# Kernel optimization log

Hardware: AMD Instinct MI355X
Metric: run time of the kernel (lower is better)

## Reference

```python
import jax, jax.numpy as jnp
import numpy as np

B, N, CQ, CKV, CP = 4, 1024, 128, 64, 16
H, NB = 4, 3
D = CQ // H  # 32 per-head dim
NQ, NK = 32, 128
CENTRES = 15.5 + 32.0 * np.arange(N // NQ)  # subset centres covering all atoms


def _ln(x, eps=1e-5):
    m = jnp.mean(x, axis=-1, keepdims=True)
    v = jnp.var(x, axis=-1, keepdims=True)
    return (x - m) * jax.lax.rsqrt(v + eps)


def _adaln(a, s, s_gamma, w_gate, w_skip):
    # AF3 AdaLN: a normalized without affine, modulated by conditioning s
    a_n = _ln(a)
    s_n = _ln(s) * s_gamma
    return jax.nn.sigmoid(s_n @ w_gate) * a_n + s_n @ w_skip


def _local_bias():
    # sequence-local block mask (union over subset centres), Algorithm 7
    idx = jnp.arange(N, dtype=jnp.float32)
    cen = jnp.asarray(CENTRES, dtype=jnp.float32)
    lcond = jnp.abs(idx[None, :] - cen[:, None]) < NQ / 2  # [C, N] query window
    mcond = jnp.abs(idx[None, :] - cen[:, None]) < NK / 2  # [C, N] key window
    cond = jnp.any(lcond[:, :, None] & mcond[:, None, :], axis=0)  # [N, N]
    return jnp.where(cond, 0.0, -1e10)


def _forward(q, c, p, attn_s_gamma, attn_gate_w, attn_skip_w, attn_wq, attn_bq,
             attn_wk, attn_wv, attn_lnz_g, attn_lnz_b, attn_wb, attn_wgate,
             attn_wo, attn_ws_out, attn_bs_out, trans_s_gamma, trans_gate_w,
             trans_skip_w, trans_w1, trans_w2, trans_wout, trans_ws_out,
             trans_bs_out):
    beta = _local_bias()  # [N, N]
    inv_sqrt_d = 1.0 / np.sqrt(D)
    a = q
    for i in range(NB):  # 3 structurally distinct blocks
        # --- AttentionPairBias (AF3 Alg 24) ---
        ah = _adaln(a, c, attn_s_gamma[i], attn_gate_w[i], attn_skip_w[i])
        qh = (ah @ attn_wq[i] + attn_bq[i]).reshape(B, N, H, D)
        kh = (ah @ attn_wk[i]).reshape(B, N, H, D)
        vh = (ah @ attn_wv[i]).reshape(B, N, H, D)
        zb = (_ln(p) * attn_lnz_g[i] + attn_lnz_b[i]) @ attn_wb[i]  # [B,N,N,H]
        bias = jnp.transpose(zb, (0, 3, 1, 2)) + beta[None, None]  # [B,H,N,N]
        scores = jnp.einsum('bqhd,bkhd->bhqk', qh, kh) * inv_sqrt_d + bias
        w = jax.nn.softmax(scores, axis=-1)
        o = jnp.einsum('bhqk,bkhd->bqhd', w, vh)
        g = jax.nn.sigmoid((ah @ attn_wgate[i]).reshape(B, N, H, D))
        o = (g * o).reshape(B, N, CQ) @ attn_wo[i]
        attn_out = jax.nn.sigmoid(c @ attn_ws_out[i] + attn_bs_out[i]) * o
        # --- ConditionedTransitionBlock (AF3 Alg 25, n=2 SwiGLU) ---
        t = _adaln(a, c, trans_s_gamma[i], trans_gate_w[i], trans_skip_w[i])
        bm = jax.nn.silu(t @ trans_w1[i]) * (t @ trans_w2[i])
        t_out = jax.nn.sigmoid(c @ trans_ws_out[i] + trans_bs_out[i]) * (bm @ trans_wout[i])
        # AF3 Alg 23: a <- attn_out + transition(a, s)
        a = attn_out + t_out
    return a


def setup_inputs() -> dict:
    key = jax.random.key(0)
    ks = iter(jax.random.split(key, 64))

    def rnd(shape, scale=0.02):
        return jax.random.normal(next(ks), shape, dtype=jnp.float32) * scale

    return {
        'q': jax.random.normal(next(ks), (B, N, CQ), dtype=jnp.float32),
        'c': jax.random.normal(next(ks), (B, N, CKV), dtype=jnp.float32),
        'p': jax.random.normal(next(ks), (B, N, N, CP), dtype=jnp.float32),
        'attn_s_gamma': jnp.ones((NB, CKV), jnp.float32),
        'attn_gate_w': rnd((NB, CKV, CQ)),
        'attn_skip_w': rnd((NB, CKV, CQ)),
        'attn_wq': rnd((NB, CQ, CQ)),
        'attn_bq': jnp.zeros((NB, CQ), jnp.float32),
        'attn_wk': rnd((NB, CQ, CQ)),
        'attn_wv': rnd((NB, CQ, CQ)),
        'attn_lnz_g': jnp.ones((NB, CP), jnp.float32),
        'attn_lnz_b': jnp.zeros((NB, CP), jnp.float32),
        'attn_wb': rnd((NB, CP, H)),
        'attn_wgate': rnd((NB, CQ, CQ)),
        'attn_wo': rnd((NB, CQ, CQ)),
        'attn_ws_out': rnd((NB, CKV, CQ)),
        'attn_bs_out': jnp.full((NB, CQ), -2.0, jnp.float32),
        'trans_s_gamma': jnp.ones((NB, CKV), jnp.float32),
        'trans_gate_w': rnd((NB, CKV, CQ)),
        'trans_skip_w': rnd((NB, CKV, CQ)),
        'trans_w1': rnd((NB, CQ, 2 * CQ)),
        'trans_w2': rnd((NB, CQ, 2 * CQ)),
        'trans_wout': rnd((NB, 2 * CQ, CQ)),
        'trans_ws_out': rnd((NB, CKV, CQ)),
        'trans_bs_out': jnp.full((NB, CQ), -2.0, jnp.float32),
    }


def reference(q, c, p, attn_s_gamma, attn_gate_w, attn_skip_w, attn_wq, attn_bq,
              attn_wk, attn_wv, attn_lnz_g, attn_lnz_b, attn_wb, attn_wgate,
              attn_wo, attn_ws_out, attn_bs_out, trans_s_gamma, trans_gate_w,
              trans_skip_w, trans_w1, trans_w2, trans_wout, trans_ws_out,
              trans_bs_out):
    return _forward(q, c, p, attn_s_gamma, attn_gate_w, attn_skip_w, attn_wq,
                    attn_bq, attn_wk, attn_wv, attn_lnz_g, attn_lnz_b, attn_wb,
                    attn_wgate, attn_wo, attn_ws_out, attn_bs_out,
                    trans_s_gamma, trans_gate_w, trans_skip_w, trans_w1,
                    trans_w2, trans_wout, trans_ws_out, trans_bs_out)
```

## Files before the change

### kernel.cpp

```cpp
#include <hip/hip_runtime.h>
#include <math.h>

#define NB_ 3
#define B_ 4
#define N_ 1024
#define CQ_ 128
#define CKV_ 64
#define CP_ 16
#define H_ 4
#define D_ 32
#define R_ (B_*N_)
#define KW_ 128

__device__ __forceinline__ float sigmoidf_(float x) {
    return 1.0f / (1.0f + __expf(-x));
}

#define AN_OFF 0
#define SA_OFF 1056
#define ST_OFF 1600
#define CR_OFF 2144
#define TH_OFF 2688
#define SCR_OFF 3744
#define SMEM_F (3744 + 6336)

__device__ __forceinline__ void pre_body(
    float2 av, float* smem, int base,
    const float* __restrict__ c,
    const float* __restrict__ a_sg, const float* __restrict__ a_gw,
    const float* __restrict__ a_sw, const float* __restrict__ a_wso,
    const float* __restrict__ a_bso,
    const float* __restrict__ t_sg, const float* __restrict__ t_gw,
    const float* __restrict__ t_sw, const float* __restrict__ t_wso,
    const float* __restrict__ t_bso,
    const float* __restrict__ wq, const float* __restrict__ bq,
    const float* __restrict__ wk, const float* __restrict__ wv,
    const float* __restrict__ wg,
    const float* __restrict__ w1, const float* __restrict__ w2,
    float* __restrict__ qh, float* __restrict__ kh,
    float* __restrict__ vh, float* __restrict__ gh,
    float* __restrict__ bm,
    float* __restrict__ asig, float* __restrict__ tsig)
{
    const int t = threadIdx.x;
    {
        const int rloc = t >> 6, li = t & 63;
        const int row = base + rloc;
        float s = av.x + av.y;
        float ss = av.x * av.x + av.y * av.y;
        float cv = c[row * 64 + li];
        float cs = cv, css = cv * cv;
        #pragma unroll
        for (int m = 1; m < 64; m <<= 1) {
            s += __shfl_xor(s, m);
            ss += __shfl_xor(ss, m);
            cs += __shfl_xor(cs, m);
            css += __shfl_xor(css, m);
        }
        const float am = s * (1.0f / 128.0f);
        const float ars = rsqrtf(ss * (1.0f / 128.0f) - am * am + 1e-5f);
        const float cm = cs * (1.0f / 64.0f);
        const float crs = rsqrtf(css * (1.0f / 64.0f) - cm * cm + 1e-5f);
        smem[AN_OFF + rloc * 132 + li * 2]     = (av.x - am) * ars;
        smem[AN_OFF + rloc * 132 + li * 2 + 1] = (av.y - am) * ars;
        const float cn = (cv - cm) * crs;
        smem[SA_OFF + rloc * 68 + li] = cn * a_sg[li];
        smem[ST_OFF + rloc * 68 + li] = cn * t_sg[li];
        smem[CR_OFF + rloc * 68 + li] = cv;
    }
    __syncthreads();

    const int wave = t >> 6;
    const int lane = t & 63;
    const int ig = lane >> 4;
    const int jc = lane & 15;
    const int c0 = jc * 8;
    const int r0 = ig * 2, r1 = ig * 2 + 1;

    if (wave < 6) {
        const float* W;
        const float* xs;
        switch (wave) {
            case 0: W = a_gw;  xs = smem + SA_OFF; break;
            case 1: W = a_sw;  xs = smem + SA_OFF; break;
            case 2: W = t_gw;  xs = smem + ST_OFF; break;
            case 3: W = t_sw;  xs = smem + ST_OFF; break;
            case 4: W = a_wso; xs = smem + CR_OFF; break;
            default: W = t_wso; xs = smem + CR_OFF; break;
        }
        W += c0;
        float acc0[8], acc1[8];
        #pragma unroll
        for (int e = 0; e < 8; e++) { acc0[e] = 0.f; acc1[e] = 0.f; }
        for (int kk = 0; kk < 64; kk += 4) {
            float4 x40 = *(const float4*)(xs + r0 * 68 + kk);
            float4 x41 = *(const float4*)(xs + r1 * 68 + kk);
            #pragma unroll
            for (int qq = 0; qq < 4; qq++) {
                const float4 wlo = *(const float4*)(W + (kk + qq) * 128);
                const float4 whi = *(const float4*)(W + (kk + qq) * 128 + 4);
                const float xa = ((const float*)&x40)[qq];
                const float xb = ((const float*)&x41)[qq];
                acc0[0] += xa * wlo.x; acc0[1] += xa * wlo.y;
                acc0[2] += xa * wlo.z; acc0[3] += xa * wlo.w;
                acc0[4] += xa * whi.x; acc0[5] += xa * whi.y;
                acc0[6] += xa * whi.z; acc0[7] += xa * whi.w;
                acc1[0] += xb * wlo.x; acc1[1] += xb * wlo.y;
                acc1[2] += xb * wlo.z; acc1[3] += xb * wlo.w;
                acc1[4] += xb * whi.x; acc1[5] += xb * whi.y;
                acc1[6] += xb * whi.z; acc1[7] += xb * whi.w;
            }
        }
        float* sc = smem + SCR_OFF + wave * 1056;
        *(float4*)(sc + r0 * 132 + c0)     = make_float4(acc0[0], acc0[1], acc0[2], acc0[3]);
        *(float4*)(sc + r0 * 132 + c0 + 4) = make_float4(acc0[4], acc0[5], acc0[6], acc0[7]);
        *(float4*)(sc + r1 * 132 + c0)     = make_float4(acc1[0], acc1[1], acc1[2], acc1[3]);
        *(float4*)(sc + r1 * 132 + c0 + 4) = make_float4(acc1[4], acc1[5], acc1[6], acc1[7]);
    }
    __syncthreads();

    #pragma unroll
    for (int i2 = 0; i2 < 2; i2++) {
        const int e = t + i2 * 512;
        const int r = e >> 7, cc = e & 127;
        const float* sc = smem + SCR_OFF + r * 132 + cc;
        const float anv = smem[AN_OFF + r * 132 + cc];
        const float ahv = sigmoidf_(sc[0]) * anv + sc[1056];
        const float thv = sigmoidf_(sc[2 * 1056]) * anv + sc[3 * 1056];
        smem[AN_OFF + r * 132 + cc] = ahv;
        smem[TH_OFF + r * 132 + cc] = thv;
        const int idx = (base + r) * 128 + cc;
        asig[idx] = sigmoidf_(sc[4 * 1056] + a_bso[cc]);
        tsig[idx] = sigmoidf_(sc[5 * 1056] + t_bso[cc]);
    }
    __syncthreads();

    {
        const float* W;
        const float* xs;
        int ldw, sel2 = 0, cb = 0;
        if (wave < 4) {
            W = (wave == 0 ? wq : wave == 1 ? wk : wave == 2 ? wv : wg) + c0;
            xs = smem + AN_OFF;
            ldw = 128;
        } else {
            const int u = (wave - 4) * 128 + c0;
            sel2 = u >> 8; cb = u & 255;
            W = (sel2 ? w2 : w1) + cb;
            xs = smem + TH_OFF;
            ldw = 256;
        }
        float acc0[8], acc1[8];
        #pragma unroll
        for (int e = 0; e < 8; e++) {
            const float init = (wave == 0) ? bq[c0 + e] : 0.f;
            acc0[e] = init; acc1[e] = init;
        }
        for (int kk = 0; kk < 128; kk += 4) {
            float4 x40 = *(const float4*)(xs + r0 * 132 + kk);
            float4 x41 = *(const float4*)(xs + r1 * 132 + kk);
            #pragma unroll
            for (int qq = 0; qq < 4; qq++) {
                const float4 wlo = *(const float4*)(W + (kk + qq) * ldw);
                const float4 whi = *(const float4*)(W + (kk + qq) * ldw + 4);
                const float xa = ((const float*)&x40)[qq];
                const float xb = ((const float*)&x41)[qq];
                acc0[0] += xa * wlo.x; acc0[1] += xa * wlo.y;
                acc0[2] += xa * wlo.z; acc0[3] += xa * wlo.w;
                acc0[4] += xa * whi.x; acc0[5] += xa * whi.y;
                acc0[6] += xa * whi.z; acc0[7] += xa * whi.w;
                acc1[0] += xb * wlo.x; acc1[1] += xb * wlo.y;
                acc1[2] += xb * wlo.z; acc1[3] += xb * wlo.w;
                acc1[4] += xb * whi.x; acc1[5] += xb * whi.y;
                acc1[6] += xb * whi.z; acc1[7] += xb * whi.w;
            }
        }
        if (wave < 4) {
            float* dst = (wave == 0 ? qh : wave == 1 ? kh : wave == 2 ? vh : gh);
            if (wave == 3) {
                #pragma unroll
                for (int e = 0; e < 8; e++) {
                    acc0[e] = sigmoidf_(acc0[e]);
                    acc1[e] = sigmoidf_(acc1[e]);
                }
            }
            *(float4*)(dst + (base + r0) * 128 + c0)     = make_float4(acc0[0], acc0[1], acc0[2], acc0[3]);
            *(float4*)(dst + (base + r0) * 128 + c0 + 4) = make_float4(acc0[4], acc0[5], acc0[6], acc0[7]);
            *(float4*)(dst + (base + r1) * 128 + c0)     = make_float4(acc1[0], acc1[1], acc1[2], acc1[3]);
            *(float4*)(dst + (base + r1) * 128 + c0 + 4) = make_float4(acc1[4], acc1[5], acc1[6], acc1[7]);
        } else {
            float* bsc = smem + SCR_OFF + sel2 * 2080;
            *(float4*)(bsc + r0 * 260 + cb)     = make_float4(acc0[0], acc0[1], acc0[2], acc0[3]);
            *(float4*)(bsc + r0 * 260 + cb + 4) = make_float4(acc0[4], acc0[5], acc0[6], acc0[7]);
            *(float4*)(bsc + r1 * 260 + cb)     = make_float4(acc1[0], acc1[1], acc1[2], acc1[3]);
            *(float4*)(bsc + r1 * 260 + cb + 4) = make_float4(acc1[4], acc1[5], acc1[6], acc1[7]);
        }
    }
    __syncthreads();

    #pragma unroll
    for (int i2 = 0; i2 < 4; i2++) {
        const int e = t + i2 * 512;
        const int r = e >> 8, cc = e & 255;
        const float a1 = smem[SCR_OFF + r * 260 + cc];
        const float a2 = smem[SCR_OFF + 2080 + r * 260 + cc];
        bm[(base + r) * 256 + cc] = a1 * sigmoidf_(a1) * a2;
    }
}

__global__ __launch_bounds__(512, 4) void k_pre0(
    const float* __restrict__ a, const float* __restrict__ c,
    const float* __restrict__ p,
    const float* __restrict__ lnz_g, const float* __restrict__ lnz_b,
    const float* __restrict__ wb, float* __restrict__ zb,
    const float* __restrict__ a_sg, const float* __restrict__ a_gw,
    const float* __restrict__ a_sw, const float* __restrict__ a_wso,
    const float* __restrict__ a_bso,
    const float* __restrict__ t_sg, const float* __restrict__ t_gw,
    const float* __restrict__ t_sw, const float* __restrict__ t_wso,
    const float* __restrict__ t_bso,
    const float* __restrict__ wq, const float* __restrict__ bq,
    const float* __restrict__ wk, const float* __restrict__ wv,
    const float* __restrict__ wg,
    const float* __restrict__ w1, const float* __restrict__ w2,
    float* __restrict__ qh, float* __restrict__ kh,
    float* __restrict__ vh, float* __restrict__ gh,
    float* __restrict__ bm,
    float* __restrict__ asig, float* __restrict__ tsig)
{
    __shared__ float smem[SMEM_F];
    const int t = threadIdx.x;
    const int base = blockIdx.x * 8;

    #pragma unroll
    for (int i = 0; i < 2; i++) {
        const int e = t + i * 512;
        const int r = e >> 7, kk = e & 127;
        const int row = base + r;
        const int n = row & 1023;
        const int k = ((n >> 5) << 5) - 48 + kk;
        if (k < 0 || k >= N_) {
            #pragma unroll
            for (int blk = 0; blk < NB_; blk++) {
                float* zo = zb + ((size_t)(blk * R_ + row) * H_) * KW_ + kk;
                #pragma unroll
                for (int h = 0; h < H_; h++) zo[h * KW_] = -1e10f;
            }
        } else {
            const float* pp = p + ((size_t)row * N_ + k) * CP_;
            float pv[16];
            float4 p0 = *(const float4*)(pp);
            float4 p1 = *(const float4*)(pp + 4);
            float4 p2 = *(const float4*)(pp + 8);
            float4 p3 = *(const float4*)(pp + 12);
            pv[0]=p0.x; pv[1]=p0.y; pv[2]=p0.z; pv[3]=p0.w;
            pv[4]=p1.x; pv[5]=p1.y; pv[6]=p1.z; pv[7]=p1.w;
            pv[8]=p2.x; pv[9]=p2.y; pv[10]=p2.z; pv[11]=p2.w;
            pv[12]=p3.x; pv[13]=p3.y; pv[14]=p3.z; pv[15]=p3.w;
            float s = 0.f, ss = 0.f;
            #pragma unroll
            for (int ii = 0; ii < 16; ii++) { s += pv[ii]; ss += pv[ii] * pv[ii]; }
            const float m = s * (1.0f / 16.0f);
            const float rs = rsqrtf(ss * (1.0f / 16.0f) - m * m + 1e-5f);
            #pragma unroll
            for (int blk = 0; blk < NB_; blk++) {
                const float* g = lnz_g + blk * 16;
                const float* bb = lnz_b + blk * 16;
                const float* w = wb + blk * 64;
                float z0 = 0.f, z1 = 0.f, z2 = 0.f, z3 = 0.f;
                #pragma unroll
                for (int cp = 0; cp < 16; cp++) {
                    const float val = (pv[cp] - m) * rs * g[cp] + bb[cp];
                    z0 += val * w[cp * 4 + 0];
                    z1 += val * w[cp * 4 + 1];
                    z2 += val * w[cp * 4 + 2];
                    z3 += val * w[cp * 4 + 3];
                }
                float* zo = zb + ((size_t)(blk * R_ + row) * H_) * KW_ + kk;
                zo[0] = z0; zo[KW_] = z1; zo[2 * KW_] = z2; zo[3 * KW_] = z3;
            }
        }
    }

    float2 av = *(const float2*)(a + (base + (t >> 6)) * 128 + (t & 63) * 2);
    pre_body(av, smem, base, c, a_sg, a_gw, a_sw, a_wso, a_bso,
             t_sg, t_gw, t_sw, t_wso, t_bso, wq, bq, wk, wv, wg, w1, w2,
             qh, kh, vh, gh, bm, asig, tsig);
}

__global__ __launch_bounds__(512, 4) void k_cp(
    const float* __restrict__ og, const float* __restrict__ bm_in,
    const float* __restrict__ wo, const float* __restrict__ wout,
    const float* __restrict__ asig_in, const float* __restrict__ tsig_in,
    float* __restrict__ out_final, int final_,
    const float* __restrict__ c,
    const float* __restrict__ a_sg, const float* __restrict__ a_gw,
    const float* __restrict__ a_sw, const float* __restrict__ a_wso,
    const float* __restrict__ a_bso,
    const float* __restrict__ t_sg, const float* __restrict__ t_gw,
    const float* __restrict__ t_sw, const float* __restrict__ t_wso,
    const float* __restrict__ t_bso,
    const float* __restrict__ wq, const float* __restrict__ bq,
    const float* __restrict__ wk, const float* __restrict__ wv,
    const float* __restrict__ wg,
    const float* __restrict__ w1, const float* __restrict__ w2,
    float* __restrict__ qh, float* __restrict__ kh,
    float* __restrict__ vh, float* __restrict__ gh,
    float* __restrict__ bm,
    float* __restrict__ asig, float* __restrict__ tsig)
{
    __shared__ float smem[SMEM_F];
    float* ogs = smem + SCR_OFF;
    float* bms = smem + SCR_OFF + 1056;
    const int t = threadIdx.x;
    const int base = blockIdx.x * 8;

    if (t < 256) {
        const int r = t >> 5, c4 = t & 31;
        *(float4*)(ogs + r * 132 + c4 * 4) =
            *(const float4*)(og + (base + r) * 128 + c4 * 4);
    }
    {
        const int r = t >> 6, c4 = t & 63;
        *(float4*)(bms + r * 260 + c4 * 4) =
            *(const float4*)(bm_in + (base + r) * 256 + c4 * 4);
    }
    __syncthreads();

    const int w = t >> 6, l = t & 63;
    const int row = base + w;
    float2 acc1 = make_float2(0.f, 0.f), acc2 = make_float2(0.f, 0.f);
    for (int k = 0; k < 128; k++) {
        const float x = ogs[w * 132 + k];
        const float2 wv = *(const float2*)(wo + k * 128 + l * 2);
        acc1.x += x * wv.x; acc1.y += x * wv.y;
    }
    for (int k = 0; k < 256; k++) {
        const float x = bms[w * 260 + k];
        const float2 wv = *(const float2*)(wout + k * 128 + l * 2);
        acc2.x += x * wv.x; acc2.y += x * wv.y;
    }
    const float2 as = *(const float2*)(asig_in + row * 128 + l * 2);
    const float2 ts = *(const float2*)(tsig_in + row * 128 + l * 2);
    float2 outv;
    outv.x = as.x * acc1.x + ts.x * acc2.x;
    outv.y = as.y * acc1.y + ts.y * acc2.y;

    if (final_) {
        *(float2*)(out_final + row * 128 + l * 2) = outv;
        return;
    }
    pre_body(outv, smem, base, c, a_sg, a_gw, a_sw, a_wso, a_bso,
             t_sg, t_gw, t_sw, t_wso, t_bso, wq, bq, wk, wv, wg, w1, w2,
             qh, kh, vh, gh, bm, asig, tsig);
}

__global__ __launch_bounds__(512, 4) void k_attn(
    const float* __restrict__ qh, const float* __restrict__ kh,
    const float* __restrict__ vh, const float* __restrict__ gh,
    const float* __restrict__ zb, float* __restrict__ og)
{
    __shared__ float qs[32 * 36];
    __shared__ float kT[32 * 136];
    __shared__ float vs[128 * 36];
    __shared__ float wsm[32 * 132];

    const int t = threadIdx.x;
    const int qb = blockIdx.x & 31;
    const int h = (blockIdx.x >> 5) & 3;
    const int b = blockIdx.x >> 7;
    const int k0 = qb * 32 - 48;

    #pragma unroll
    for (int i = 0; i < 2; i++) {
        const int e = t + i * 512;
        const int kk = e >> 3, dq = e & 7;
        const int kg = k0 + kk;
        float4 kv = make_float4(0.f, 0.f, 0.f, 0.f);
        float4 vv = make_float4(0.f, 0.f, 0.f, 0.f);
        if (kg >= 0 && kg < N_) {
            const int addr = (b * N_ + kg) * 128 + h * 32 + dq * 4;
            kv = *(const float4*)(kh + addr);
            vv = *(const float4*)(vh + addr);
        }
        kT[(dq * 4 + 0) * 136 + kk] = kv.x;
        kT[(dq * 4 + 1) * 136 + kk] = kv.y;
        kT[(dq * 4 + 2) * 136 + kk] = kv.z;
        kT[(dq * 4 + 3) * 136 + kk] = kv.w;
        *(float4*)(vs + kk * 36 + dq * 4) = vv;
    }
    if (t < 256) {
        const int q = t >> 3, dq = t & 7;
        const int n = qb * 32 + q;
        *(float4*)(qs + q * 36 + dq * 4) =
            *(const float4*)(qh + (b * N_ + n) * 128 + h * 32 + dq * 4);
    }
    const int q = t >> 4, jj = t & 15;
    const int n = qb * 32 + q;
    const float* zrow = zb + ((size_t)(b * N_ + n) * H_ + h) * KW_;
    const float4 z0 = *(const float4*)(zrow + jj * 8);
    const float4 z1 = *(const float4*)(zrow + jj * 8 + 4);
    __syncthreads();

    float acc[8];
    #pragma unroll
    for (int e = 0; e < 8; e++) acc[e] = 0.f;
    for (int d = 0; d < 32; d++) {
        const float qv = qs[q * 36 + d];
        const float4 ka = *(const float4*)(kT + d * 136 + jj * 8);
        const float4 kb = *(const float4*)(kT + d * 136 + jj * 8 + 4);
        acc[0] += qv * ka.x; acc[1] += qv * ka.y;
        acc[2] += qv * ka.z; acc[3] += qv * ka.w;
        acc[4] += qv * kb.x; acc[5] += qv * kb.y;
        acc[6] += qv * kb.z; acc[7] += qv * kb.w;
    }
    const float scale = 0.1767766952966369f;
    float fr[8];
    fr[0] = acc[0] * scale + z0.x; fr[1] = acc[1] * scale + z0.y;
    fr[2] = acc[2] * scale + z0.z; fr[3] = acc[3] * scale + z0.w;
    fr[4] = acc[4] * scale + z1.x; fr[5] = acc[5] * scale + z1.y;
    fr[6] = acc[6] * scale + z1.z; fr[7] = acc[7] * scale + z1.w;
    float mx = fr[0];
    #pragma unroll
    for (int i = 1; i < 8; i++) mx = fmaxf(mx, fr[i]);
    #pragma unroll
    for (int mk = 1; mk < 16; mk <<= 1) mx = fmaxf(mx, __shfl_xor(mx, mk));
    float sum = 0.f;
    #pragma unroll
    for (int i = 0; i < 8; i++) { fr[i] = __expf(fr[i] - mx); sum += fr[i]; }
    #pragma unroll
    for (int mk = 1; mk < 16; mk <<= 1) sum += __shfl_xor(sum, mk);
    const float rinv = 1.0f / sum;
    #pragma unroll
    for (int i = 0; i < 8; i++)
        wsm[q * 132 + jj * 8 + i] = fr[i] * rinv;
    __syncthreads();

    const int q2 = t >> 4, dq2 = (t >> 1) & 7, kh2 = t & 1;
    float4 o = make_float4(0.f, 0.f, 0.f, 0.f);
    const int kbeg = kh2 * 64;
    for (int kk = kbeg; kk < kbeg + 64; kk++) {
        const float wv = wsm[q2 * 132 + kk];
        const float4 v4 = *(const float4*)(vs + kk * 36 + dq2 * 4);
        o.x += wv * v4.x; o.y += wv * v4.y;
        o.z += wv * v4.z; o.w += wv * v4.w;
    }
    o.x += __shfl_xor(o.x, 1);
    o.y += __shfl_xor(o.y, 1);
    o.z += __shfl_xor(o.z, 1);
    o.w += __shfl_xor(o.w, 1);
    if (kh2 == 0) {
        const int n2 = qb * 32 + q2;
        const int addr = (b * N_ + n2) * 128 + h * 32 + dq2 * 4;
        const float4 g4 = *(const float4*)(gh + addr);
        float4 outv;
        outv.x = o.x * g4.x; outv.y = o.y * g4.y;
        outv.z = o.z * g4.z; outv.w = o.w * g4.w;
        *(float4*)(og + addr) = outv;
    }
}

extern "C" void kernel_launch(void* const* d_in, const int* in_sizes, int n_in,
                              void* d_out, int out_size, void* d_ws, size_t ws_size,
                              hipStream_t stream)
{
    const float* q        = (const float*)d_in[0];
    const float* c        = (const float*)d_in[1];
    const float* p        = (const float*)d_in[2];
    const float* a_sg_all = (const float*)d_in[3];
    const float* a_gw_all = (const float*)d_in[4];
    const float* a_sw_all = (const float*)d_in[5];
    const float* wq_all   = (const float*)d_in[6];
    const float* bq_all   = (const float*)d_in[7];
    const float* wk_all   = (const float*)d_in[8];
    const float* wv_all   = (const float*)d_in[9];
    const float* lnzg_all = (const float*)d_in[10];
    const float* lnzb_all = (const float*)d_in[11];
    const float* wb_all   = (const float*)d_in[12];
    const float* wgt_all  = (const float*)d_in[13];
    const float* wo_all   = (const float*)d_in[14];
    const float* awso_all = (const float*)d_in[15];
    const float* abso_all = (const float*)d_in[16];
    const float* t_sg_all = (const float*)d_in[17];
    const float* t_gw_all = (const float*)d_in[18];
    const float* t_sw_all = (const float*)d_in[19];
    const float* w1_all   = (const float*)d_in[20];
    const float* w2_all   = (const float*)d_in[21];
    const float* wout_all = (const float*)d_in[22];
    const float* twso_all = (const float*)d_in[23];
    const float* tbso_all = (const float*)d_in[24];

    float* ws = (float*)d_ws;
    const size_t RC = (size_t)R_ * CQ_;
    float* qh   = ws;
    float* kh   = ws + RC;
    float* vh   = ws + 2 * RC;
    float* gh   = ws + 3 * RC;
    float* bmb  = ws + 4 * RC;
    float* asig = ws + 6 * RC;
    float* tsig = ws + 7 * RC;
    float* ogb  = ws + 8 * RC;
    float* zbb  = ws + 9 * RC;

    k_pre0<<<dim3(R_ / 8), dim3(512), 0, stream>>>(
        q, c, p, lnzg_all, lnzb_all, wb_all, zbb,
        a_sg_all, a_gw_all, a_sw_all, awso_all, abso_all,
        t_sg_all, t_gw_all, t_sw_all, twso_all, tbso_all,
        wq_all, bq_all, wk_all, wv_all, wgt_all, w1_all, w2_all,
        qh, kh, vh, gh, bmb, asig, tsig);

    for (int blk = 0; blk < NB_; blk++) {
        k_attn<<<dim3(512), dim3(512), 0, stream>>>(
            qh, kh, vh, gh, zbb + (size_t)blk * R_ * H_ * KW_, ogb);
        const int nxt = blk + 1;
        const int fin = (nxt == NB_);
        const int wi = fin ? 0 : nxt;
        k_cp<<<dim3(R_ / 8), dim3(512), 0, stream>>>(
            ogb, bmb, wo_all + blk * CQ_ * CQ_, wout_all + blk * 2 * CQ_ * CQ_,
            asig, tsig, (float*)d_out, fin,
            c,
            a_sg_all + wi * CKV_, a_gw_all + wi * CKV_ * CQ_,
            a_sw_all + wi * CKV_ * CQ_, awso_all + wi * CKV_ * CQ_,
            abso_all + wi * CQ_,
            t_sg_all + wi * CKV_, t_gw_all + wi * CKV_ * CQ_,
            t_sw_all + wi * CKV_ * CQ_, twso_all + wi * CKV_ * CQ_,
            tbso_all + wi * CQ_,
            wq_all + wi * CQ_ * CQ_, bq_all + wi * CQ_,
            wk_all + wi * CQ_ * CQ_, wv_all + wi * CQ_ * CQ_,
            wgt_all + wi * CQ_ * CQ_,
            w1_all + wi * CQ_ * 2 * CQ_, w2_all + wi * CQ_ * 2 * CQ_,
            qh, kh, vh, gh, bmb, asig, tsig);
    }
}
```

Baseline: 686.4 us.

## Fuse all stages into one persistent kernel with software grid barriers

Replaces the seven separate launches (pre, then attention and combine per block) with a single persistent kernel of 256 workgroups. The workgroups synchronise through an atomic counter used as a grid barrier, and the q/k/v/g buffers are double-buffered so the next block's projections can be written while others still read. Each workgroup now handles 16 rows and two attention tiles, and the combine GEMM splits its K dimension across waves. This removes per-launch overhead and inter-kernel gaps, but the barriers need every workgroup resident at once, and the smaller grid may lose parallelism.

```diff
diff --git a/kernel.cpp b/kernel.cpp
--- a/kernel.cpp
+++ b/kernel.cpp
@@ -8,9 +8,9 @@
 #define CKV_ 64
 #define CP_ 16
 #define H_ 4
-#define D_ 32
 #define R_ (B_*N_)
 #define KW_ 128
+#define NBLK 256
 
 __device__ __forceinline__ float sigmoidf_(float x) {
     return 1.0f / (1.0f + __expf(-x));
@@ -22,7 +22,26 @@
 #define CR_OFF 2144
 #define TH_OFF 2688
 #define SCR_OFF 3744
-#define SMEM_F (3744 + 6336)
+#define AOUT_OFF 10080
+#define QS_OFF 0
+#define KT_OFF 1152
+#define VS_OFF 5504
+#define WS_OFF 10112
+#define SMEM_F 14336
+
+__device__ __forceinline__ void grid_barrier(unsigned* bar, unsigned target) {
+    __syncthreads();
+    if (threadIdx.x == 0) {
+        __builtin_amdgcn_fence(__ATOMIC_RELEASE, "agent");
+        __hip_atomic_fetch_add(bar, 1u, __ATOMIC_ACQ_REL, __HIP_MEMORY_SCOPE_AGENT);
+        while (__hip_atomic_load(bar, __ATOMIC_RELAXED,
+                                 __HIP_MEMORY_SCOPE_AGENT) < target) {
+            __builtin_amdgcn_s_sleep(2);
+        }
+        __builtin_amdgcn_fence(__ATOMIC_ACQUIRE, "agent");
+    }
+    __syncthreads();
+}
 
 __device__ __forceinline__ void pre_body(
     float2 av, float* smem, int base,
@@ -206,37 +225,231 @@
         const float a2 = smem[SCR_OFF + 2080 + r * 260 + cc];
         bm[(base + r) * 256 + cc] = a1 * sigmoidf_(a1) * a2;
     }
+    __syncthreads();
 }
 
-__global__ __launch_bounds__(512, 4) void k_pre0(
-    const float* __restrict__ a, const float* __restrict__ c,
+__device__ __forceinline__ void attn_body(
+    float* smem, int tile,
+    const float* __restrict__ qh, const float* __restrict__ kh,
+    const float* __restrict__ vh, const float* __restrict__ gh,
+    const float* __restrict__ zb, float* __restrict__ og)
+{
+    float* qs = smem + QS_OFF;
+    float* kT = smem + KT_OFF;
+    float* vs = smem + VS_OFF;
+    float* wsm = smem + WS_OFF;
+    const int t = threadIdx.x;
+    const int qb = tile & 31;
+    const int h = (tile >> 5) & 3;
+    const int b = tile >> 7;
+    const int k0 = qb * 32 - 48;
+
+    #pragma unroll
+    for (int i = 0; i < 2; i++) {
+        const int e = t + i * 512;
+        const int kk = e >> 3, dq = e & 7;
+        const int kg = k0 + kk;
+        float4 kv = make_float4(0.f, 0.f, 0.f, 0.f);
+        float4 vv = make_float4(0.f, 0.f, 0.f, 0.f);
+        if (kg >= 0 && kg < N_) {
+            const int addr = (b * N_ + kg) * 128 + h * 32 + dq * 4;
+            kv = *(const float4*)(kh + addr);
+            vv = *(const float4*)(vh + addr);
+        }
+        kT[(dq * 4 + 0) * 136 + kk] = kv.x;
+        kT[(dq * 4 + 1) * 136 + kk] = kv.y;
+        kT[(dq * 4 + 2) * 136 + kk] = kv.z;
+        kT[(dq * 4 + 3) * 136 + kk] = kv.w;
+        *(float4*)(vs + kk * 36 + dq * 4) = vv;
+    }
+    if (t < 256) {
+        const int q = t >> 3, dq = t & 7;
+        const int n = qb * 32 + q;
+        *(float4*)(qs + q * 36 + dq * 4) =
+            *(const float4*)(qh + (b * N_ + n) * 128 + h * 32 + dq * 4);
+    }
+    const int q = t >> 4, jj = t & 15;
+    const int n = qb * 32 + q;
+    const float* zrow = zb + ((size_t)(b * N_ + n) * H_ + h) * KW_;
+    const float4 z0 = *(const float4*)(zrow + jj * 8);
+    const float4 z1 = *(const float4*)(zrow + jj * 8 + 4);
+    __syncthreads();
+
+    float acc[8];
+    #pragma unroll
+    for (int e = 0; e < 8; e++) acc[e] = 0.f;
+    for (int d = 0; d < 32; d++) {
+        const float qv = qs[q * 36 + d];
+        const float4 ka = *(const float4*)(kT + d * 136 + jj * 8);
+        const float4 kb = *(const float4*)(kT + d * 136 + jj * 8 + 4);
+        acc[0] += qv * ka.x; acc[1] += qv * ka.y;
+        acc[2] += qv * ka.z; acc[3] += qv * ka.w;
+        acc[4] += qv * kb.x; acc[5] += qv * kb.y;
+        acc[6] += qv * kb.z; acc[7] += qv * kb.w;
+    }
+    const float scale = 0.1767766952966369f;
+    float fr[8];
+    fr[0] = acc[0] * scale + z0.x; fr[1] = acc[1] * scale + z0.y;
+    fr[2] = acc[2] * scale + z0.z; fr[3] = acc[3] * scale + z0.w;
+    fr[4] = acc[4] * scale + z1.x; fr[5] = acc[5] * scale + z1.y;
+    fr[6] = acc[6] * scale + z1.z; fr[7] = acc[7] * scale + z1.w;
+    float mx = fr[0];
+    #pragma unroll
+    for (int i = 1; i < 8; i++) mx = fmaxf(mx, fr[i]);
+    #pragma unroll
+    for (int mk = 1; mk < 16; mk <<= 1) mx = fmaxf(mx, __shfl_xor(mx, mk));
+    float sum = 0.f;
+    #pragma unroll
+    for (int i = 0; i < 8; i++) { fr[i] = __expf(fr[i] - mx); sum += fr[i]; }
+    #pragma unroll
+    for (int mk = 1; mk < 16; mk <<= 1) sum += __shfl_xor(sum, mk);
+    const float rinv = 1.0f / sum;
+    #pragma unroll
+    for (int i = 0; i < 8; i++)
+        wsm[q * 132 + jj * 8 + i] = fr[i] * rinv;
+    __syncthreads();
+
+    const int q2 = t >> 4, dq2 = (t >> 1) & 7, kh2 = t & 1;
+    float4 o = make_float4(0.f, 0.f, 0.f, 0.f);
+    const int kbeg = kh2 * 64;
+    for (int kk = kbeg; kk < kbeg + 64; kk++) {
+        const float wv = wsm[q2 * 132 + kk];
+        const float4 v4 = *(const float4*)(vs + kk * 36 + dq2 * 4);
+        o.x += wv * v4.x; o.y += wv * v4.y;
+        o.z += wv * v4.z; o.w += wv * v4.w;
+    }
+    o.x += __shfl_xor(o.x, 1);
+    o.y += __shfl_xor(o.y, 1);
+    o.z += __shfl_xor(o.z, 1);
+    o.w += __shfl_xor(o.w, 1);
+    if (kh2 == 0) {
+        const int n2 = qb * 32 + q2;
+        const int addr = (b * N_ + n2) * 128 + h * 32 + dq2 * 4;
+        const float4 g4 = *(const float4*)(gh + addr);
+        float4 outv;
+        outv.x = o.x * g4.x; outv.y = o.y * g4.y;
+        outv.z = o.z * g4.z; outv.w = o.w * g4.w;
+        *(float4*)(og + addr) = outv;
+    }
+    __syncthreads();
+}
+
+__device__ __forceinline__ void combine16(
+    float* smem, int base16,
+    const float* __restrict__ og, const float* __restrict__ bmg,
+    const float* __restrict__ wo, const float* __restrict__ wout,
+    const float* __restrict__ asig, const float* __restrict__ tsig,
+    float* __restrict__ outp)
+{
+    const int t = threadIdx.x;
+    const int grp = t >> 8;
+    const int tg = t & 255;
+    const int base8 = base16 + grp * 8;
+    float* scr = smem + grp * 4224;
+    const int wave = tg >> 6, lane = tg & 63;
+    const int ig = lane >> 4, jc = lane & 15;
+    const int c0 = jc * 8;
+    const int r0 = ig * 2, r1 = ig * 2 + 1;
+
+    float acc0[8], acc1[8];
+    #pragma unroll
+    for (int e = 0; e < 8; e++) { acc0[e] = 0.f; acc1[e] = 0.f; }
+
+    if (wave < 2) {
+        const float* W = wo + c0;
+        const float* X = og + base8 * 128;
+        const int kbeg = wave * 64;
+        for (int kk = kbeg; kk < kbeg + 64; kk += 4) {
+            float4 x40 = *(const float4*)(X + r0 * 128 + kk);
+            float4 x41 = *(const float4*)(X + r1 * 128 + kk);
+            #pragma unroll
+            for (int qq = 0; qq < 4; qq++) {
+                const float4 wlo = *(const float4*)(W + (kk + qq) * 128);
+                const float4 whi = *(const float4*)(W + (kk + qq) * 128 + 4);
+                const float xa = ((const float*)&x40)[qq];
+                const float xb = ((const float*)&x41)[qq];
+                acc0[0] += xa * wlo.x; acc0[1] += xa * wlo.y;
+                acc0[2] += xa * wlo.z; acc0[3] += xa * wlo.w;
+                acc0[4] += xa * whi.x; acc0[5] += xa * whi.y;
+                acc0[6] += xa * whi.z; acc0[7] += xa * whi.w;
+                acc1[0] += xb * wlo.x; acc1[1] += xb * wlo.y;
+                acc1[2] += xb * wlo.z; acc1[3] += xb * wlo.w;
+                acc1[4] += xb * whi.x; acc1[5] += xb * whi.y;
+                acc1[6] += xb * whi.z; acc1[7] += xb * whi.w;
+            }
+        }
+    } else {
+        const float* W = wout + c0;
+        const float* X = bmg + base8 * 256;
+        const int kbeg = (wave - 2) * 128;
+        for (int kk = kbeg; kk < kbeg + 128; kk += 4) {
+            float4 x40 = *(const float4*)(X + r0 * 256 + kk);
+            float4 x41 = *(const float4*)(X + r1 * 256 + kk);
+            #pragma unroll
+            for (int qq = 0; qq < 4; qq++) {
+                const float4 wlo = *(const float4*)(W + (kk + qq) * 128);
+                const float4 whi = *(const float4*)(W + (kk + qq) * 128 + 4);
+                const float xa = ((const float*)&x40)[qq];
+                const float xb = ((const float*)&x41)[qq];
+                acc0[0] += xa * wlo.x; acc0[1] += xa * wlo.y;
+                acc0[2] += xa * wlo.z; acc0[3] += xa * wlo.w;
+                acc0[4] += xa * whi.x; acc0[5] += xa * whi.y;
+                acc0[6] += xa * whi.z; acc0[7] += xa * whi.w;
+                acc1[0] += xb * wlo.x; acc1[1] += xb * wlo.y;
+                acc1[2] += xb * wlo.z; acc1[3] += xb * wlo.w;
+                acc1[4] += xb * whi.x; acc1[5] += xb * whi.y;
+                acc1[6] += xb * whi.z; acc1[7] += xb * whi.w;
+            }
+        }
+    }
+    float* sc = scr + wave * 1056;
+    *(float4*)(sc + r0 * 132 + c0)     = make_float4(acc0[0], acc0[1], acc0[2], acc0[3]);
+    *(float4*)(sc + r0 * 132 + c0 + 4) = make_float4(acc0[4], acc0[5], acc0[6], acc0[7]);
+    *(float4*)(sc + r1 * 132 + c0)     = make_float4(acc1[0], acc1[1], acc1[2], acc1[3]);
+    *(float4*)(sc + r1 * 132 + c0 + 4) = make_float4(acc1[4], acc1[5], acc1[6], acc1[7]);
+    __syncthreads();
+
+    #pragma unroll
+    for (int i2 = 0; i2 < 4; i2++) {
+        const int e = tg + i2 * 256;
+        const int r = e >> 7, cc = e & 127;
+        const float* s = scr + r * 132 + cc;
+        const int idx = (base8 + r) * 128 + cc;
+        const float v = asig[idx] * (s[0] + s[1056]) + tsig[idx] * (s[2112] + s[3168]);
+        if (outp) outp[idx] = v;
+        else smem[AOUT_OFF + (grp * 8 + r) * 132 + cc] = v;
+    }
+    __syncthreads();
+}
+
+__global__ __launch_bounds__(512, 2) void k_mega(
+    const float* __restrict__ q, const float* __restrict__ c,
     const float* __restrict__ p,
-    const float* __restrict__ lnz_g, const float* __restrict__ lnz_b,
-    const float* __restrict__ wb, float* __restrict__ zb,
-    const float* __restrict__ a_sg, const float* __restrict__ a_gw,
-    const float* __restrict__ a_sw, const float* __restrict__ a_wso,
-    const float* __restrict__ a_bso,
-    const float* __restrict__ t_sg, const float* __restrict__ t_gw,
-    const float* __restrict__ t_sw, const float* __restrict__ t_wso,
-    const float* __restrict__ t_bso,
-    const float* __restrict__ wq, const float* __restrict__ bq,
-    const float* __restrict__ wk, const float* __restrict__ wv,
-    const float* __restrict__ wg,
-    const float* __restrict__ w1, const float* __restrict__ w2,
-    float* __restrict__ qh, float* __restrict__ kh,
-    float* __restrict__ vh, float* __restrict__ gh,
-    float* __restrict__ bm,
-    float* __restrict__ asig, float* __restrict__ tsig)
+    const float* __restrict__ a_sg_all, const float* __restrict__ a_gw_all,
+    const float* __restrict__ a_sw_all, const float* __restrict__ wq_all,
+    const float* __restrict__ bq_all, const float* __restrict__ wk_all,
+    const float* __restrict__ wv_all, const float* __restrict__ lnzg,
+    const float* __restrict__ lnzb, const float* __restrict__ wb_all,
+    const float* __restrict__ wgt_all, const float* __restrict__ wo_all,
+    const float* __restrict__ awso_all, const float* __restrict__ abso_all,
+    const float* __restrict__ t_sg_all, const float* __restrict__ t_gw_all,
+    const float* __restrict__ t_sw_all, const float* __restrict__ w1_all,
+    const float* __restrict__ w2_all, const float* __restrict__ wout_all,
+    const float* __restrict__ twso_all, const float* __restrict__ tbso_all,
+    float* qhA, float* khA, float* vhA, float* ghA,
+    float* qhB, float* khB, float* vhB, float* ghB,
+    float* ogA, float* ogB, float* bm, float* asig, float* tsig,
+    float* zb, unsigned* bar, float* out)
 {
     __shared__ float smem[SMEM_F];
     const int t = threadIdx.x;
-    const int base = blockIdx.x * 8;
-
-    #pragma unroll
-    for (int i = 0; i < 2; i++) {
+    const int base16 = blockIdx.x * 16;
+
+    #pragma unroll
+    for (int i = 0; i < 4; i++) {
         const int e = t + i * 512;
         const int r = e >> 7, kk = e & 127;
-        const int row = base + r;
+        const int row = base16 + r;
         const int n = row & 1023;
         const int k = ((n >> 5) << 5) - 48 + kk;
         if (k < 0 || k >= N_) {
@@ -264,9 +477,9 @@
             const float rs = rsqrtf(ss * (1.0f / 16.0f) - m * m + 1e-5f);
             #pragma unroll
             for (int blk = 0; blk < NB_; blk++) {
-                const float* g = lnz_g + blk * 16;
-                const float* bb = lnz_b + blk * 16;
-                const float* w = wb + blk * 64;
+                const float* g = lnzg + blk * 16;
+                const float* bb = lnzb + blk * 16;
+                const float* w = wb_all + blk * 64;
                 float z0 = 0.f, z1 = 0.f, z2 = 0.f, z3 = 0.f;
                 #pragma unroll
                 for (int cp = 0; cp < 16; cp++) {
@@ -282,181 +495,83 @@
         }
     }
 
-    float2 av = *(const float2*)(a + (base + (t >> 6)) * 128 + (t & 63) * 2);
-    pre_body(av, smem, base, c, a_sg, a_gw, a_sw, a_wso, a_bso,
-             t_sg, t_gw, t_sw, t_wso, t_bso, wq, bq, wk, wv, wg, w1, w2,
-             qh, kh, vh, gh, bm, asig, tsig);
-}
-
-__global__ __launch_bounds__(512, 4) void k_cp(
-    const float* __restrict__ og, const float* __restrict__ bm_in,
-    const float* __restrict__ wo, const float* __restrict__ wout,
-    const float* __restrict__ asig_in, const float* __restrict__ tsig_in,
-    float* __restrict__ out_final, int final_,
-    const float* __restrict__ c,
-    const float* __restrict__ a_sg, const float* __restrict__ a_gw,
-    const float* __restrict__ a_sw, const float* __restrict__ a_wso,
-    const float* __restrict__ a_bso,
-    const float* __restrict__ t_sg, const float* __restrict__ t_gw,
-    const float* __restrict__ t_sw, const float* __restrict__ t_wso,
-    const float* __restrict__ t_bso,
-    const float* __restrict__ wq, const float* __restrict__ bq,
-    const float* __restrict__ wk, const float* __restrict__ wv,
-    const float* __restrict__ wg,
-    const float* __restrict__ w1, const float* __restrict__ w2,
-    float* __restrict__ qh, float* __restrict__ kh,
-    float* __restrict__ vh, float* __restrict__ gh,
-    float* __restrict__ bm,
-    float* __restrict__ asig, float* __restrict__ tsig)
-{
-    __shared__ float smem[SMEM_F];
-    float* ogs = smem + SCR_OFF;
-    float* bms = smem + SCR_OFF + 1056;
-    const int t = threadIdx.x;
-    const int base = blockIdx.x * 8;
-
-    if (t < 256) {
-        const int r = t >> 5, c4 = t & 31;
-        *(float4*)(ogs + r * 132 + c4 * 4) =
-            *(const float4*)(og + (base + r) * 128 + c4 * 4);
-    }
     {
-        const int r = t >> 6, c4 = t & 63;
-        *(float4*)(bms + r * 260 + c4 * 4) =
-            *(const float4*)(bm_in + (base + r) * 256 + c4 * 4);
-    }
-    __syncthreads();
-
-    const int w = t >> 6, l = t & 63;
-    const int row = base + w;
-    float2 acc1 = make_float2(0.f, 0.f), acc2 = make_float2(0.f, 0.f);
-    for (int k = 0; k < 128; k++) {
-        const float x = ogs[w * 132 + k];
-        const float2 wv = *(const float2*)(wo + k * 128 + l * 2);
-        acc1.x += x * wv.x; acc1.y += x * wv.y;
-    }
-    for (int k = 0; k < 256; k++) {
-        const float x = bms[w * 260 + k];
-        const float2 wv = *(const float2*)(wout + k * 128 + l * 2);
-        acc2.x += x * wv.x; acc2.y += x * wv.y;
-    }
-    const float2 as = *(const float2*)(asig_in + row * 128 + l * 2);
-    const float2 ts = *(const float2*)(tsig_in + row * 128 + l * 2);
-    float2 outv;
-    outv.x = as.x * acc1.x + ts.x * acc2.x;
-    outv.y = as.y * acc1.y + ts.y * acc2.y;
-
-    if (final_) {
-        *(float2*)(out_final + row * 128 + l * 2) = outv;
-        return;
-    }
-    pre_body(outv, smem, base, c, a_sg, a_gw, a_sw, a_wso, a_bso,
-             t_sg, t_gw, t_sw, t_wso, t_bso, wq, bq, wk, wv, wg, w1, w2,
-             qh, kh, vh, gh, bm, asig, tsig);
-}
-
-__global__ __launch_bounds__(512, 4) void k_attn(
-    const float* __restrict__ qh, const float* __restrict__ kh,
-    const float* __restrict__ vh, const float* __restrict__ gh,
-    const float* __restrict__ zb, float* __restrict__ og)
-{
-    __shared__ float qs[32 * 36];
-    __shared__ float kT[32 * 136];
-    __shared__ float vs[128 * 36];
-    __shared__ float wsm[32 * 132];
-
-    const int t = threadIdx.x;
-    const int qb = blockIdx.x & 31;
-    const int h = (blockIdx.x >> 5) & 3;
-    const int b = blockIdx.x >> 7;
-    const int k0 = qb * 32 - 48;
-
-    #pragma unroll
-    for (int i = 0; i < 2; i++) {
-        const int e = t + i * 512;
-        const int kk = e >> 3, dq = e & 7;
-        const int kg = k0 + kk;
-        float4 kv = make_float4(0.f, 0.f, 0.f, 0.f);
-        float4 vv = make_float4(0.f, 0.f, 0.f, 0.f);
-        if (kg >= 0 && kg < N_) {
-            const int addr = (b * N_ + kg) * 128 + h * 32 + dq * 4;
-            kv = *(const float4*)(kh + addr);
-            vv = *(const float4*)(vh + addr);
-        }
-        kT[(dq * 4 + 0) * 136 + kk] = kv.x;
-        kT[(dq * 4 + 1) * 136 + kk] = kv.y;
-        kT[(dq * 4 + 2) * 136 + kk] = kv.z;
-        kT[(dq * 4 + 3) * 136 + kk] = kv.w;
-        *(float4*)(vs + kk * 36 + dq * 4) = vv;
-    }
-    if (t < 256) {
-        const int q = t >> 3, dq = t & 7;
-        const int n = qb * 32 + q;
-        *(float4*)(qs + q * 36 + dq * 4) =
-            *(const float4*)(qh + (b * N_ + n) * 128 + h * 32 + dq * 4);
-    }
-    const int q = t >> 4, jj = t & 15;
-    const int n = qb * 32 + q;
-    const float* zrow = zb + ((size_t)(b * N_ + n) * H_ + h) * KW_;
-    const float4 z0 = *(const float4*)(zrow + jj * 8);
-    const float4 z1 = *(const float4*)(zrow + jj * 8 + 4);
-    __syncthreads();
-
-    float acc[8];
-    #pragma unroll
-    for (int e = 0; e < 8; e++) acc[e] = 0.f;
-    for (int d = 0; d < 32; d++) {
-        const float qv = qs[q * 36 + d];
-        const float4 ka = *(const float4*)(kT + d * 136 + jj * 8);
-        const float4 kb = *(const float4*)(kT + d * 136 + jj * 8 + 4);
-        acc[0] += qv * ka.x; acc[1] += qv * ka.y;
-        acc[2] += qv * ka.z; acc[3] += qv * ka.w;
-        acc[4] += qv * kb.x; acc[5] += qv * kb.y;
-        acc[6] += qv * kb.z; acc[7] += qv * kb.w;
-    }
-    const float scale = 0.1767766952966369f;
-    float fr[8];
-    fr[0] = acc[0] * scale + z0.x; fr[1] = acc[1] * scale + z0.y;
-    fr[2] = acc[2] * scale + z0.z; fr[3] = acc[3] * scale + z0.w;
-    fr[4] = acc[4] * scale + z1.x; fr[5] = acc[5] * scale + z1.y;
-    fr[6] = acc[6] * scale + z1.z; fr[7] = acc[7] * scale + z1.w;
-    float mx = fr[0];
-    #pragma unroll
-    for (int i = 1; i < 8; i++) mx = fmaxf(mx, fr[i]);
-    #pragma unroll
-    for (int mk = 1; mk < 16; mk <<= 1) mx = fmaxf(mx, __shfl_xor(mx, mk));
-    float sum = 0.f;
-    #pragma unroll
-    for (int i = 0; i < 8; i++) { fr[i] = __expf(fr[i] - mx); sum += fr[i]; }
-    #pragma unroll
-    for (int mk = 1; mk < 16; mk <<= 1) sum += __shfl_xor(sum, mk);
-    const float rinv = 1.0f / sum;
-    #pragma unroll
-    for (int i = 0; i < 8; i++)
-        wsm[q * 132 + jj * 8 + i] = fr[i] * rinv;
-    __syncthreads();
-
-    const int q2 = t >> 4, dq2 = (t >> 1) & 7, kh2 = t & 1;
-    float4 o = make_float4(0.f, 0.f, 0.f, 0.f);
-    const int kbeg = kh2 * 64;
-    for (int kk = kbeg; kk < kbeg + 64; kk++) {
-        const float wv = wsm[q2 * 132 + kk];
-        const float4 v4 = *(const float4*)(vs + kk * 36 + dq2 * 4);
-        o.x += wv * v4.x; o.y += wv * v4.y;
-        o.z += wv * v4.z; o.w += wv * v4.w;
-    }
-    o.x += __shfl_xor(o.x, 1);
-    o.y += __shfl_xor(o.y, 1);
-    o.z += __shfl_xor(o.z, 1);
-    o.w += __shfl_xor(o.w, 1);
-    if (kh2 == 0) {
-        const int n2 = qb * 32 + q2;
-        const int addr = (b * N_ + n2) * 128 + h * 32 + dq2 * 4;
-        const float4 g4 = *(const float4*)(gh + addr);
-        float4 outv;
-        outv.x = o.x * g4.x; outv.y = o.y * g4.y;
-        outv.z = o.z * g4.z; outv.w = o.w * g4.w;
-        *(float4*)(og + addr) = outv;
+        float2 av0 = *(const float2*)(q + (base16 + (t >> 6)) * 128 + (t & 63) * 2);
+        float2 av1 = *(const float2*)(q + (base16 + 8 + (t >> 6)) * 128 + (t & 63) * 2);
+        pre_body(av0, smem, base16, c,
+                 a_sg_all, a_gw_all, a_sw_all, awso_all, abso_all,
+                 t_sg_all, t_gw_all, t_sw_all, twso_all, tbso_all,
+                 wq_all, bq_all, wk_all, wv_all, wgt_all, w1_all, w2_all,
+                 qhA, khA, vhA, ghA, bm, asig, tsig);
+        pre_body(av1, smem, base16 + 8, c,
+                 a_sg_all, a_gw_all, a_sw_all, awso_all, abso_all,
+                 t_sg_all, t_gw_all, t_sw_all, twso_all, tbso_all,
+                 wq_all, bq_all, wk_all, wv_all, wgt_all, w1_all, w2_all,
+                 qhA, khA, vhA, ghA, bm, asig, tsig);
+    }
+
+    unsigned phase = 0;
+    for (int blk = 0; blk < NB_; blk++) {
+        const int pb = blk & 1;
+        const float* qh = pb ? qhB : qhA;
+        const float* kh = pb ? khB : khA;
+        const float* vh = pb ? vhB : vhA;
+        const float* gh = pb ? ghB : ghA;
+        float* og = pb ? ogB : ogA;
+
+        phase++;
+        grid_barrier(bar, phase * NBLK);
+
+        const float* zbl = zb + (size_t)blk * R_ * H_ * KW_;
+        attn_body(smem, blockIdx.x * 2 + 0, qh, kh, vh, gh, zbl, og);
+        attn_body(smem, blockIdx.x * 2 + 1, qh, kh, vh, gh, zbl, og);
+
+        phase++;
+        grid_barrier(bar, phase * NBLK);
+
+        const int fin = (blk == NB_ - 1);
+        combine16(smem, base16, og, bm,
+                  wo_all + blk * CQ_ * CQ_, wout_all + blk * 2 * CQ_ * CQ_,
+                  asig, tsig, fin ? out : nullptr);
+
+        if (!fin) {
+            const int nb = blk + 1;
+            float* nqh = (nb & 1) ? qhB : qhA;
+            float* nkh = (nb & 1) ? khB : khA;
+            float* nvh = (nb & 1) ? vhB : vhA;
+            float* ngh = (nb & 1) ? ghB : ghA;
+            const int rl = t >> 6, li2 = (t & 63) * 2;
+            float2 av0, av1;
+            av0.x = smem[AOUT_OFF + rl * 132 + li2];
+            av0.y = smem[AOUT_OFF + rl * 132 + li2 + 1];
+            av1.x = smem[AOUT_OFF + (8 + rl) * 132 + li2];
+            av1.y = smem[AOUT_OFF + (8 + rl) * 132 + li2 + 1];
+            __syncthreads();
+            pre_body(av0, smem, base16, c,
+                     a_sg_all + nb * CKV_, a_gw_all + nb * CKV_ * CQ_,
+                     a_sw_all + nb * CKV_ * CQ_, awso_all + nb * CKV_ * CQ_,
+                     abso_all + nb * CQ_,
+                     t_sg_all + nb * CKV_, t_gw_all + nb * CKV_ * CQ_,
+                     t_sw_all + nb * CKV_ * CQ_, twso_all + nb * CKV_ * CQ_,
+                     tbso_all + nb * CQ_,
+                     wq_all + nb * CQ_ * CQ_, bq_all + nb * CQ_,
+                     wk_all + nb * CQ_ * CQ_, wv_all + nb * CQ_ * CQ_,
+                     wgt_all + nb * CQ_ * CQ_,
+                     w1_all + nb * CQ_ * 2 * CQ_, w2_all + nb * CQ_ * 2 * CQ_,
+                     nqh, nkh, nvh, ngh, bm, asig, tsig);
+            pre_body(av1, smem, base16 + 8, c,
+                     a_sg_all + nb * CKV_, a_gw_all + nb * CKV_ * CQ_,
+                     a_sw_all + nb * CKV_ * CQ_, awso_all + nb * CKV_ * CQ_,
+                     abso_all + nb * CQ_,
+                     t_sg_all + nb * CKV_, t_gw_all + nb * CKV_ * CQ_,
+                     t_sw_all + nb * CKV_ * CQ_, twso_all + nb * CKV_ * CQ_,
+                     tbso_all + nb * CQ_,
+                     wq_all + nb * CQ_ * CQ_, bq_all + nb * CQ_,
+                     wk_all + nb * CQ_ * CQ_, wv_all + nb * CQ_ * CQ_,
+                     wgt_all + nb * CQ_ * CQ_,
+                     w1_all + nb * CQ_ * 2 * CQ_, w2_all + nb * CQ_ * 2 * CQ_,
+                     nqh, nkh, nvh, ngh, bm, asig, tsig);
+        }
     }
 }
 
@@ -492,43 +607,30 @@
 
     float* ws = (float*)d_ws;
     const size_t RC = (size_t)R_ * CQ_;
-    float* qh   = ws;
-    float* kh   = ws + RC;
-    float* vh   = ws + 2 * RC;
-    float* gh   = ws + 3 * RC;
-    float* bmb  = ws + 4 * RC;
-    float* asig = ws + 6 * RC;
-    float* tsig = ws + 7 * RC;
-    float* ogb  = ws + 8 * RC;
-    float* zbb  = ws + 9 * RC;
-
-    k_pre0<<<dim3(R_ / 8), dim3(512), 0, stream>>>(
-        q, c, p, lnzg_all, lnzb_all, wb_all, zbb,
-        a_sg_all, a_gw_all, a_sw_all, awso_all, abso_all,
-        t_sg_all, t_gw_all, t_sw_all, twso_all, tbso_all,
-        wq_all, bq_all, wk_all, wv_all, wgt_all, w1_all, w2_all,
-        qh, kh, vh, gh, bmb, asig, tsig);
-
-    for (int blk = 0; blk < NB_; blk++) {
-        k_attn<<<dim3(512), dim3(512), 0, stream>>>(
-            qh, kh, vh, gh, zbb + (size_t)blk * R_ * H_ * KW_, ogb);
-        const int nxt = blk + 1;
-        const int fin = (nxt == NB_);
-        const int wi = fin ? 0 : nxt;
-        k_cp<<<dim3(R_ / 8), dim3(512), 0, stream>>>(
-            ogb, bmb, wo_all + blk * CQ_ * CQ_, wout_all + blk * 2 * CQ_ * CQ_,
-            asig, tsig, (float*)d_out, fin,
-            c,
-            a_sg_all + wi * CKV_, a_gw_all + wi * CKV_ * CQ_,
-            a_sw_all + wi * CKV_ * CQ_, awso_all + wi * CKV_ * CQ_,
-            abso_all + wi * CQ_,
-            t_sg_all + wi * CKV_, t_gw_all + wi * CKV_ * CQ_,
-            t_sw_all + wi * CKV_ * CQ_, twso_all + wi * CKV_ * CQ_,
-            tbso_all + wi * CQ_,
-            wq_all + wi * CQ_ * CQ_, bq_all + wi * CQ_,
-            wk_all + wi * CQ_ * CQ_, wv_all + wi * CQ_ * CQ_,
-            wgt_all + wi * CQ_ * CQ_,
-            w1_all + wi * CQ_ * 2 * CQ_, w2_all + wi * CQ_ * 2 * CQ_,
-            qh, kh, vh, gh, bmb, asig, tsig);
-    }
+    float* qhA  = ws;
+    float* khA  = ws + RC;
+    float* vhA  = ws + 2 * RC;
+    float* ghA  = ws + 3 * RC;
+    float* qhB  = ws + 4 * RC;
+    float* khB  = ws + 5 * RC;
+    float* vhB  = ws + 6 * RC;
+    float* ghB  = ws + 7 * RC;
+    float* ogA  = ws + 8 * RC;
+    float* ogB  = ws + 9 * RC;
+    float* bm   = ws + 10 * RC;
+    float* asig = ws + 12 * RC;
+    float* tsig = ws + 13 * RC;
+    float* zbb  = ws + 14 * RC;
+    unsigned* bar = (unsigned*)(ws + 26 * RC);
+
+    hipMemsetAsync(bar, 0, 256, stream);
+
+    k_mega<<<dim3(NBLK), dim3(512), 0, stream>>>(
+        q, c, p,
+        a_sg_all, a_gw_all, a_sw_all, wq_all, bq_all, wk_all, wv_all,
+        lnzg_all, lnzb_all, wb_all, wgt_all, wo_all, awso_all, abso_all,
+        t_sg_all, t_gw_all, t_sw_all, w1_all, w2_all, wout_all,
+        twso_all, tbso_all,
+        qhA, khA, vhA, ghA, qhB, khB, vhB, ghB,
+        ogA, ogB, bm, asig, tsig, zbb, bar, (float*)d_out);
 }
```

Result: slower. 742.2 us (+8.1%).
